# Kernel optimization log

Measured on AMD Instinct MI355X. Metric: run time of the kernel, lower is better.

## Reference

```python
import jax, jax.numpy as jnp
import numpy as np

B, H, E, G, SEQ_LEN = 131072, 64, 16, 32, 30


def setup_inputs() -> dict:
    key = jax.random.key(0)
    ks = jax.random.split(key, 17)
    def lin(kw, kb, out_f, in_f):
        s = 1.0 / np.sqrt(in_f)
        W = jax.random.uniform(kw, (out_f, in_f), jnp.float32, -s, s)
        b = jax.random.uniform(kb, (out_f,), jnp.float32, -s, s)
        return W, b
    W_se, b_se = lin(ks[0], ks[1], E, 2)
    W_h2p, b_h2p = lin(ks[2], ks[3], 2, 3 * H)
    W_goal, b_goal = lin(ks[4], ks[5], H, 2 * G)
    W_abs, b_abs = lin(ks[6], ks[7], H, 2)
    W_ih, b_ih = lin(ks[8], ks[9], 4 * H, E)
    W_hh, b_hh = lin(ks[10], ks[11], 4 * H, H)
    return {
        "traj_abs": jax.random.normal(ks[12], (1, B, 2), jnp.float32),
        "traj_rel": jax.random.normal(ks[13], (1, B, 2), jnp.float32),
        "h0": jax.random.normal(ks[14], (1, B, H), jnp.float32),
        "c0": jax.random.normal(ks[15], (1, B, H), jnp.float32),
        "goals": jax.random.normal(ks[16], (B, G, 2), jnp.float32),
        "W_ih": W_ih, "W_hh": W_hh, "b_ih": b_ih, "b_hh": b_hh,
        "W_se": W_se, "b_se": b_se,
        "W_h2p": W_h2p, "b_h2p": b_h2p,
        "W_goal": W_goal, "b_goal": b_goal,
        "W_abs": W_abs, "b_abs": b_abs,
    }


def reference(traj_abs, traj_rel, h0, c0, goals,
              W_ih, W_hh, b_ih, b_hh,
              W_se, b_se, W_h2p, b_h2p,
              W_goal, b_goal, W_abs, b_abs):
    b = traj_abs.shape[1]
    goal_emb = goals.reshape(b, -1) @ W_goal.T + b_goal            # (b, H)
    dec_in = jax.nn.leaky_relu(traj_rel[0] @ W_se.T + b_se)        # (b, E)

    def step(carry, _):
        h, c, x, abs_pos = carry
        gates = x @ W_ih.T + b_ih + h @ W_hh.T + b_hh              # (b, 4H)
        i, f, g, o = jnp.split(gates, 4, axis=-1)                  # PyTorch gate order
        c = jax.nn.sigmoid(f) * c + jax.nn.sigmoid(i) * jnp.tanh(g)
        h = jax.nn.sigmoid(o) * jnp.tanh(c)
        abs_emb = abs_pos @ W_abs.T + b_abs                        # (b, H)
        inp = jnp.concatenate([h, abs_emb, goal_emb], axis=1)      # (b, 3H)
        rel = inp @ W_h2p.T + b_h2p                                # (b, 2)
        x = jax.nn.leaky_relu(rel @ W_se.T + b_se)
        return (h, c, x, abs_pos + rel), rel

    _, rels = jax.lax.scan(step, (h0[0], c0[0], dec_in, traj_abs[0]),
                           None, length=SEQ_LEN)
    return rels  # (seq_len, b, 2)
```

## Files before the change

kernel.cpp:

```cpp
#include <hip/hip_runtime.h>
#include <stdint.h>


#define B_TOT 131072
#define SEQL 30
#define WPB 8

typedef _Float16 f16x8 __attribute__((ext_vector_type(8)));
typedef _Float16 f16x2 __attribute__((ext_vector_type(2)));
typedef float f32x4 __attribute__((ext_vector_type(4)));
typedef float f32x2 __attribute__((ext_vector_type(2)));

__device__ __forceinline__ float fexp2(float x) {
#if __has_builtin(__builtin_amdgcn_exp2f)
  return __builtin_amdgcn_exp2f(x);
#else
  return exp2f(x);
#endif
}
__device__ __forceinline__ float frcp(float x) {
#if __has_builtin(__builtin_amdgcn_rcpf)
  return __builtin_amdgcn_rcpf(x);
#else
  return 1.0f / x;
#endif
}

__global__ void setup_consts(const float* __restrict__ Wgoal,
                             const float* __restrict__ bgoal,
                             const float* __restrict__ Wh2p,
                             const float* __restrict__ bh2p,
                             const float* __restrict__ Wabs,
                             const float* __restrict__ babs,
                             float* __restrict__ wsf) {
  const int tid = threadIdx.x;
  const int wv = tid >> 6;
  const int lane = tid & 63;
  if (wv == 0) {
    const int k = lane;
    float s0 = 0.f, s1 = 0.f;
#pragma unroll 8
    for (int jj = 0; jj < 64; ++jj) {
      float wg = Wgoal[jj * 64 + k];
      s0 += wg * Wh2p[128 + jj];
      s1 += wg * Wh2p[320 + jj];
    }
    wsf[k] = s0;
    wsf[64 + k] = s1;
  } else {
    const int i = lane >> 3, sub = lane & 7;
    const int p = i & 1, grp = i >> 1;
    float s = 0.f;
#pragma unroll
    for (int t = 0; t < 8; ++t) {
      int j = sub * 8 + t;
      float wv_ = (grp < 3) ? Wh2p[p * 192 + 64 + j] : Wh2p[p * 192 + 128 + j];
      float av = (grp == 0)   ? Wabs[j * 2 + 0]
                 : (grp == 1) ? Wabs[j * 2 + 1]
                 : (grp == 2) ? babs[j]
                              : bgoal[j];
      s += av * wv_;
    }
    s += __shfl_xor(s, 1, 64);
    s += __shfl_xor(s, 2, 64);
    s += __shfl_xor(s, 4, 64);
    if (sub == 0) {
      if (grp == 2) s += bh2p[p];
      wsf[128 + i] = s;
    }
  }
}

__global__ __launch_bounds__(512, 4) void lstm_mfma(
    const float* __restrict__ tabs, const float* __restrict__ trel,
    const float* __restrict__ h0, const float* __restrict__ c0,
    const float* __restrict__ goals, const float* __restrict__ Wih,
    const float* __restrict__ Whh, const float* __restrict__ bih,
    const float* __restrict__ bhh, const float* __restrict__ Wse,
    const float* __restrict__ bse, const float* __restrict__ Wh2p,
    const float* __restrict__ wsf, float* __restrict__ outp) {
  const int lane = threadIdx.x & 63;
  const int w = threadIdx.x >> 6;
  const int q = lane >> 4;
  const int n = lane & 15;
  const int pm = n & 3;
  const int bb = blockIdx.x * (16 * WPB) + 16 * w;

  __shared__ __align__(16) _Float16 whh[4 * 64 * 64];
  __shared__ __align__(16) _Float16 wx[4 * 64 * 32];
  __shared__ __align__(16) _Float16 hscr[WPB * 16 * 64];

  const float SI = -1.4426950408889634f;
  const float SG = 2.8853900817779268f;

  for (int idx = threadIdx.x; idx < 4 * 64 * 64; idx += 512) {
    const int r = idx >> 6, k = idx & 63;
    const float sc = ((r >> 6) == 2) ? SG : SI;
    const int slot = (k >> 3) ^ (r & 7);
    whh[r * 64 + slot * 8 + (k & 7)] = (_Float16)(sc * Whh[r * 64 + k]);
  }
  if (threadIdx.x < 256) {
    const int r = threadIdx.x;
    const float sc = ((r >> 6) == 2) ? SG : SI;
    float bfold = 0.f, m20 = 0.f, m21 = 0.f;
#pragma unroll
    for (int k = 0; k < 16; ++k) {
      float wik = Wih[r * 16 + k];
      bfold += bse[k] * wik;
      m20 += Wse[k * 2 + 0] * wik;
      m21 += Wse[k * 2 + 1] * wik;
    }
    const float bias = sc * (bih[r] + bhh[r] + 0.505f * bfold);
#pragma unroll
    for (int kx = 0; kx < 32; ++kx) {
      float v;
      if (kx < 16)
        v = sc * Wih[r * 16 + kx];
      else if (kx == 16)
        v = bias;
      else if (kx == 17)
        v = sc * 0.505f * m20;
      else if (kx == 18)
        v = sc * 0.505f * m21;
      else
        v = 0.f;
      const int slot = (kx >> 3) ^ (r & 3);
      wx[r * 32 + slot * 8 + (kx & 7)] = (_Float16)v;
    }
  }

  f16x8 awp0, awp1;
#pragma unroll
  for (int j = 0; j < 8; ++j) {
    float v0 = (pm < 2) ? Wh2p[pm * 192 + q * 8 + j] : 0.f;
    float v1 = (pm < 2) ? Wh2p[pm * 192 + 32 + q * 8 + j] : 0.f;
    awp0[j] = (_Float16)v0;
    awp1[j] = (_Float16)v1;
  }
  const float Sx0 = wsf[128], Sx1 = wsf[129];
  const float Sy0 = wsf[130], Sy1 = wsf[131];

  f16x2 wsaP[4], wsbP[4], bscP[4];
  const uint32_t xmask = (q < 2) ? 0x7FFF7FFFu : 0xFFFFFFFFu;
#pragma unroll
  for (int jj = 0; jj < 4; ++jj) {
    f16x2 z = f16x2{(_Float16)0.f, (_Float16)0.f};
    if (q < 2) {
      int kx = q * 8 + 2 * jj;
      wsaP[jj] = f16x2{(_Float16)(0.495f * Wse[kx * 2 + 0]),
                       (_Float16)(0.495f * Wse[kx * 2 + 2])};
      wsbP[jj] = f16x2{(_Float16)(0.495f * Wse[kx * 2 + 1]),
                       (_Float16)(0.495f * Wse[kx * 2 + 3])};
      bscP[jj] = f16x2{(_Float16)(0.495f * bse[kx]),
                       (_Float16)(0.495f * bse[kx + 1])};
    } else if (q == 2 && jj == 0) {
      wsaP[jj] = f16x2{(_Float16)0.f, (_Float16)1.f};
      wsbP[jj] = z;
      bscP[jj] = f16x2{(_Float16)1.f, (_Float16)0.f};
    } else if (q == 2 && jj == 1) {
      wsaP[jj] = z;
      wsbP[jj] = f16x2{(_Float16)1.f, (_Float16)0.f};
      bscP[jj] = z;
    } else {
      wsaP[jj] = z;
      wsbP[jj] = z;
      bscP[jj] = z;
    }
  }

  auto build_x = [&](float r0f, float r1f) -> f16x8 {
    f16x2 r0h = f16x2{(_Float16)r0f, (_Float16)r0f};
    f16x2 r1h = f16x2{(_Float16)r1f, (_Float16)r1f};
    f16x8 xr;
#pragma unroll
    for (int jj = 0; jj < 4; ++jj) {
      f16x2 t = r0h * wsaP[jj] + (r1h * wsbP[jj] + bscP[jj]);
      uint32_t tu = __builtin_bit_cast(uint32_t, t) & xmask;
      f16x2 lr = __builtin_bit_cast(f16x2, tu);
      xr[2 * jj] = lr[0];
      xr[2 * jj + 1] = lr[1];
    }
    return xr;
  };

  const f32x4 zC = {0.f, 0.f, 0.f, 0.f};
  const int wbase = w * 1024;

  float Gg0, Gg1, ax, ay;
  float cst[4][4];
  f16x8 xf;
  {
    f16x8 aM0, aM1, bg0, bg1;
#pragma unroll
    for (int j = 0; j < 8; ++j) {
      int k = q * 8 + j;
      aM0[j] = (_Float16)((pm < 2) ? wsf[pm * 64 + k] : 0.f);
      aM1[j] = (_Float16)((pm < 2) ? wsf[pm * 64 + 32 + k] : 0.f);
      bg0[j] = (_Float16)goals[(bb + n) * 64 + k];
      bg1[j] = (_Float16)goals[(bb + n) * 64 + 32 + k];
    }
    f32x4 Ga = __builtin_amdgcn_mfma_f32_16x16x32_f16(aM0, bg0, zC, 0, 0, 0);
    Ga = __builtin_amdgcn_mfma_f32_16x16x32_f16(aM1, bg1, Ga, 0, 0, 0);
    Gg0 = Ga[0] + wsf[132] + wsf[134];
    Gg1 = Ga[1] + wsf[133] + wsf[135];

    ax = tabs[(bb + n) * 2 + 0];
    ay = tabs[(bb + n) * 2 + 1];
#pragma unroll
    for (int m = 0; m < 4; ++m) {
      const int c16 = 2 * m + (n >> 3);
#pragma unroll
      for (int r = 0; r < 4; ++r) {
        const int br = 4 * q + r;
        cst[m][r] = c0[(bb + br) * 64 + 16 * m + n];
        hscr[wbase + br * 64 + ((c16 ^ (br & 7)) << 3) + (n & 7)] =
            (_Float16)h0[(bb + br) * 64 + 16 * m + n];
      }
    }
    xf = build_x(trel[(bb + n) * 2 + 0], trel[(bb + n) * 2 + 1]);
  }

  __syncthreads();

  const int ro0 = wbase + n * 64 + ((q ^ (n & 7)) << 3);
  const int ro1 = wbase + n * 64 + (((4 + q) ^ (n & 7)) << 3);
  const int sl0 = (q ^ (n & 7)) << 3;
  const int sl1 = ((4 + q) ^ (n & 7)) << 3;
  const int xsl = (q ^ (n & 3)) << 3;
  const float K2 = 2.8853900817779268f;

  for (int s = 0; s <= SEQL; ++s) {
    const f16x8 ah0 = *(const f16x8*)(hscr + ro0);
    const f16x8 ah1 = *(const f16x8*)(hscr + ro1);

    if (s > 0) {
      f32x4 p = __builtin_amdgcn_mfma_f32_16x16x32_f16(awp0, ah0, zC, 0, 0, 0);
      p = __builtin_amdgcn_mfma_f32_16x16x32_f16(awp1, ah1, p, 0, 0, 0);
      float u0 = p[0] + Gg0 + fmaf(ax, Sx0, ay * Sy0);
      float u1 = p[1] + Gg1 + fmaf(ax, Sx1, ay * Sy1);
      ax += u0;
      ay += u1;
      if (lane < 16) {
        float2 v;
        v.x = u0;
        v.y = u1;
        ((float2*)outp)[(size_t)(s - 1) * B_TOT + bb + lane] = v;
      }
      xf = build_x(u0, u1);
    }

    if (s < SEQL) {
#pragma unroll
      for (int m = 0; m < 4; ++m) {
        const int hb = (16 * m + n) * 64;
        const int xb = (16 * m + n) * 32 + xsl;
        f32x4 acc[4];
#pragma unroll
        for (int g = 0; g < 4; ++g) {
          const f16x8 w0 = *(const f16x8*)(whh + g * 4096 + hb + sl0);
          const f16x8 w1 = *(const f16x8*)(whh + g * 4096 + hb + sl1);
          const f16x8 w2 = *(const f16x8*)(wx + g * 2048 + xb);
          f32x4 a = __builtin_amdgcn_mfma_f32_16x16x32_f16(ah0, w0, zC,
                                                           0, 0, 0);
          a = __builtin_amdgcn_mfma_f32_16x16x32_f16(ah1, w1, a, 0, 0, 0);
          a = __builtin_amdgcn_mfma_f32_16x16x32_f16(xf, w2, a, 0, 0, 0);
          acc[g] = a;
        }
        const int c16 = 2 * m + (n >> 3);
#pragma unroll
        for (int pr = 0; pr < 2; ++pr) {
          const int ra = 2 * pr, rb = 2 * pr + 1;
          f32x2 Av = {fexp2(acc[0][ra]), fexp2(acc[0][rb])};
          f32x2 Fv = {fexp2(acc[1][ra]), fexp2(acc[1][rb])};
          f32x2 Bv = {fexp2(acc[2][ra]), fexp2(acc[2][rb])};
          const f32x2 one = {1.f, 1.f};
          f32x2 t1 = Av + one;
          f32x2 t2 = Bv + one;
          f32x2 t3 = Fv + one;
          f32x2 t4 = Bv - one;
          f32x2 m1 = t1 * t2;
          f32x2 cs = {cst[m][ra], cst[m][rb]};
          f32x2 num = cs * m1 + t4 * t3;
          f32x2 den = m1 * t3;
          float Rc = frcp(den[0] * den[1]);
          float cc0 = num[0] * den[1] * Rc;
          float cc1 = num[1] * den[0] * Rc;
          cst[m][ra] = cc0;
          cst[m][rb] = cc1;
          f32x2 Cv = {fexp2(acc[3][ra]), fexp2(acc[3][rb])};
          f32x2 Dv = {fexp2(K2 * cc0), fexp2(K2 * cc1)};
          f32x2 hd = (Cv + one) * (Dv + one);
          f32x2 hnm = Dv - one;
          float Rh = frcp(hd[0] * hd[1]);
          float h0v = hnm[0] * hd[1] * Rh;
          float h1v = hnm[1] * hd[0] * Rh;
          const int bra = 4 * q + ra, brb = 4 * q + rb;
          hscr[wbase + bra * 64 + ((c16 ^ (bra & 7)) << 3) + (n & 7)] =
              (_Float16)h0v;
          hscr[wbase + brb * 64 + ((c16 ^ (brb & 7)) << 3) + (n & 7)] =
              (_Float16)h1v;
        }
      }
    }
  }
}

extern "C" void kernel_launch(void* const* d_in, const int* in_sizes, int n_in,
                              void* d_out, int out_size, void* d_ws,
                              size_t ws_size, hipStream_t stream) {
  (void)in_sizes; (void)n_in; (void)out_size; (void)ws_size;
  const float* tabs  = (const float*)d_in[0];
  const float* trel  = (const float*)d_in[1];
  const float* h0    = (const float*)d_in[2];
  const float* c0    = (const float*)d_in[3];
  const float* goals = (const float*)d_in[4];
  const float* Wih   = (const float*)d_in[5];
  const float* Whh   = (const float*)d_in[6];
  const float* bih   = (const float*)d_in[7];
  const float* bhh   = (const float*)d_in[8];
  const float* Wse   = (const float*)d_in[9];
  const float* bse   = (const float*)d_in[10];
  const float* Wh2p  = (const float*)d_in[11];
  const float* bh2p  = (const float*)d_in[12];
  const float* Wgoal = (const float*)d_in[13];
  const float* bgoal = (const float*)d_in[14];
  const float* Wabs  = (const float*)d_in[15];
  const float* babs  = (const float*)d_in[16];
  float* wsf = (float*)d_ws;

  setup_consts<<<dim3(1), dim3(128), 0, stream>>>(Wgoal, bgoal, Wh2p, bh2p,
                                                  Wabs, babs, wsf);
  lstm_mfma<<<dim3(B_TOT / (16 * WPB)), dim3(512), 0, stream>>>(
      tabs, trel, h0, c0, goals, Wih, Whh, bih, bhh, Wse, bse, Wh2p, wsf,
      (float*)d_out);
}
```

Before: 447.4 us.

## Pre-swizzle weights into MFMA fragment order and transpose gate MFMA operands

Stores the LSTM recurrent and input weights in shared memory already laid out as per-lane MFMA B-fragments, so each lane loads its operand with one contiguous 16-byte read and no XOR swizzle addressing. The gate MFMAs swap operand order so each lane's accumulator holds consecutive hidden units for one batch row. That lets the new h be packed into f16x4 and written with one vector store instead of scalar 16-bit stores. h0 and c0 are now loaded with vectorized contiguous reads, at the cost of a new, bank-conflict-sensitive shared-memory layout for hscr.

```diff
diff --git a/kernel.cpp b/kernel.cpp
--- a/kernel.cpp
+++ b/kernel.cpp
@@ -7,6 +7,7 @@
 #define WPB 8
 
 typedef _Float16 f16x8 __attribute__((ext_vector_type(8)));
+typedef _Float16 f16x4 __attribute__((ext_vector_type(4)));
 typedef _Float16 f16x2 __attribute__((ext_vector_type(2)));
 typedef float f32x4 __attribute__((ext_vector_type(4)));
 typedef float f32x2 __attribute__((ext_vector_type(2)));
@@ -86,47 +87,50 @@
   const int pm = n & 3;
   const int bb = blockIdx.x * (16 * WPB) + 16 * w;
 
-  __shared__ __align__(16) _Float16 whh[4 * 64 * 64];
-  __shared__ __align__(16) _Float16 wx[4 * 64 * 32];
-  __shared__ __align__(16) _Float16 hscr[WPB * 16 * 64];
+  __shared__ __align__(16) _Float16 wfrag[48 * 512];
+  __shared__ __align__(16) _Float16 hscr[WPB * 2 * 512];
 
   const float SI = -1.4426950408889634f;
   const float SG = 2.8853900817779268f;
 
-  for (int idx = threadIdx.x; idx < 4 * 64 * 64; idx += 512) {
-    const int r = idx >> 6, k = idx & 63;
-    const float sc = ((r >> 6) == 2) ? SG : SI;
-    const int slot = (k >> 3) ^ (r & 7);
-    whh[r * 64 + slot * 8 + (k & 7)] = (_Float16)(sc * Whh[r * 64 + k]);
-  }
-  if (threadIdx.x < 256) {
-    const int r = threadIdx.x;
-    const float sc = ((r >> 6) == 2) ? SG : SI;
-    float bfold = 0.f, m20 = 0.f, m21 = 0.f;
-#pragma unroll
-    for (int k = 0; k < 16; ++k) {
-      float wik = Wih[r * 16 + k];
-      bfold += bse[k] * wik;
-      m20 += Wse[k * 2 + 0] * wik;
-      m21 += Wse[k * 2 + 1] * wik;
-    }
-    const float bias = sc * (bih[r] + bhh[r] + 0.505f * bfold);
-#pragma unroll
-    for (int kx = 0; kx < 32; ++kx) {
-      float v;
-      if (kx < 16)
-        v = sc * Wih[r * 16 + kx];
-      else if (kx == 16)
-        v = bias;
-      else if (kx == 17)
-        v = sc * 0.505f * m20;
-      else if (kx == 18)
-        v = sc * 0.505f * m21;
-      else
-        v = 0.f;
-      const int slot = (kx >> 3) ^ (r & 3);
-      wx[r * 32 + slot * 8 + (kx & 7)] = (_Float16)v;
-    }
+  for (int f = (int)(threadIdx.x >> 6); f < 48; f += 8) {
+    const int which = f % 3, gs = f / 3;
+    const int g = gs >> 2, s = gs & 3;
+    const int row = g * 64 + 16 * s + n;
+    const float sc = (g == 2) ? SG : SI;
+    f16x8 v;
+    if (which < 2) {
+#pragma unroll
+      for (int j = 0; j < 8; ++j)
+        v[j] = (_Float16)(sc * Whh[row * 64 + which * 32 + 8 * q + j]);
+    } else {
+      float bfold = 0.f, m20 = 0.f, m21 = 0.f;
+#pragma unroll
+      for (int k = 0; k < 16; ++k) {
+        float wik = Wih[row * 16 + k];
+        bfold += bse[k] * wik;
+        m20 += Wse[k * 2 + 0] * wik;
+        m21 += Wse[k * 2 + 1] * wik;
+      }
+      const float bias = sc * (bih[row] + bhh[row] + 0.505f * bfold);
+#pragma unroll
+      for (int j = 0; j < 8; ++j) {
+        const int kx = 8 * q + j;
+        float vv;
+        if (kx < 16)
+          vv = sc * Wih[row * 16 + kx];
+        else if (kx == 16)
+          vv = bias;
+        else if (kx == 17)
+          vv = sc * 0.505f * m20;
+        else if (kx == 18)
+          vv = sc * 0.505f * m21;
+        else
+          vv = 0.f;
+        v[j] = (_Float16)vv;
+      }
+    }
+    *(f16x8*)(wfrag + f * 512 + lane * 8) = v;
   }
 
   f16x8 awp0, awp1;
@@ -184,7 +188,7 @@
   };
 
   const f32x4 zC = {0.f, 0.f, 0.f, 0.f};
-  const int wbase = w * 1024;
+  const int wb = w * 1024;
 
   float Gg0, Gg1, ax, ay;
   float cst[4][4];
@@ -207,31 +211,34 @@
     ax = tabs[(bb + n) * 2 + 0];
     ay = tabs[(bb + n) * 2 + 1];
 #pragma unroll
-    for (int m = 0; m < 4; ++m) {
-      const int c16 = 2 * m + (n >> 3);
-#pragma unroll
-      for (int r = 0; r < 4; ++r) {
-        const int br = 4 * q + r;
-        cst[m][r] = c0[(bb + br) * 64 + 16 * m + n];
-        hscr[wbase + br * 64 + ((c16 ^ (br & 7)) << 3) + (n & 7)] =
-            (_Float16)h0[(bb + br) * 64 + 16 * m + n];
-      }
+    for (int t = 0; t < 2; ++t) {
+      f16x8 hv;
+#pragma unroll
+      for (int j = 0; j < 8; ++j)
+        hv[j] = (_Float16)h0[(bb + n) * 64 + 32 * t + 8 * q + j];
+      *(f16x8*)(hscr + wb + t * 512 + lane * 8) = hv;
+    }
+#pragma unroll
+    for (int s4 = 0; s4 < 4; ++s4) {
+      const float4 cv =
+          *(const float4*)(c0 + (size_t)(bb + n) * 64 + 16 * s4 + 4 * q);
+      cst[s4][0] = cv.x;
+      cst[s4][1] = cv.y;
+      cst[s4][2] = cv.z;
+      cst[s4][3] = cv.w;
     }
     xf = build_x(trel[(bb + n) * 2 + 0], trel[(bb + n) * 2 + 1]);
   }
 
   __syncthreads();
 
-  const int ro0 = wbase + n * 64 + ((q ^ (n & 7)) << 3);
-  const int ro1 = wbase + n * 64 + (((4 + q) ^ (n & 7)) << 3);
-  const int sl0 = (q ^ (n & 7)) << 3;
-  const int sl1 = ((4 + q) ^ (n & 7)) << 3;
-  const int xsl = (q ^ (n & 3)) << 3;
+  const _Float16* wfp = wfrag + lane * 8;
+  const int wwo = wb + 128 * (q >> 1) + 8 * n + 4 * (q & 1);
   const float K2 = 2.8853900817779268f;
 
   for (int s = 0; s <= SEQL; ++s) {
-    const f16x8 ah0 = *(const f16x8*)(hscr + ro0);
-    const f16x8 ah1 = *(const f16x8*)(hscr + ro1);
+    const f16x8 ah0 = *(const f16x8*)(hscr + wb + lane * 8);
+    const f16x8 ah1 = *(const f16x8*)(hscr + wb + 512 + lane * 8);
 
     if (s > 0) {
       f32x4 p = __builtin_amdgcn_mfma_f32_16x16x32_f16(awp0, ah0, zC, 0, 0, 0);
@@ -251,22 +258,20 @@
 
     if (s < SEQL) {
 #pragma unroll
-      for (int m = 0; m < 4; ++m) {
-        const int hb = (16 * m + n) * 64;
-        const int xb = (16 * m + n) * 32 + xsl;
+      for (int s4 = 0; s4 < 4; ++s4) {
         f32x4 acc[4];
 #pragma unroll
         for (int g = 0; g < 4; ++g) {
-          const f16x8 w0 = *(const f16x8*)(whh + g * 4096 + hb + sl0);
-          const f16x8 w1 = *(const f16x8*)(whh + g * 4096 + hb + sl1);
-          const f16x8 w2 = *(const f16x8*)(wx + g * 2048 + xb);
-          f32x4 a = __builtin_amdgcn_mfma_f32_16x16x32_f16(ah0, w0, zC,
+          const f16x8 w0 = *(const f16x8*)(wfp + (12 * g + 3 * s4 + 0) * 512);
+          const f16x8 w1 = *(const f16x8*)(wfp + (12 * g + 3 * s4 + 1) * 512);
+          const f16x8 w2 = *(const f16x8*)(wfp + (12 * g + 3 * s4 + 2) * 512);
+          f32x4 a = __builtin_amdgcn_mfma_f32_16x16x32_f16(w0, ah0, zC,
                                                            0, 0, 0);
-          a = __builtin_amdgcn_mfma_f32_16x16x32_f16(ah1, w1, a, 0, 0, 0);
-          a = __builtin_amdgcn_mfma_f32_16x16x32_f16(xf, w2, a, 0, 0, 0);
+          a = __builtin_amdgcn_mfma_f32_16x16x32_f16(w1, ah1, a, 0, 0, 0);
+          a = __builtin_amdgcn_mfma_f32_16x16x32_f16(w2, xf, a, 0, 0, 0);
           acc[g] = a;
         }
-        const int c16 = 2 * m + (n >> 3);
+        f16x4 hp;
 #pragma unroll
         for (int pr = 0; pr < 2; ++pr) {
           const int ra = 2 * pr, rb = 2 * pr + 1;
@@ -279,27 +284,23 @@
           f32x2 t3 = Fv + one;
           f32x2 t4 = Bv - one;
           f32x2 m1 = t1 * t2;
-          f32x2 cs = {cst[m][ra], cst[m][rb]};
+          f32x2 cs = {cst[s4][ra], cst[s4][rb]};
           f32x2 num = cs * m1 + t4 * t3;
           f32x2 den = m1 * t3;
           float Rc = frcp(den[0] * den[1]);
           float cc0 = num[0] * den[1] * Rc;
           float cc1 = num[1] * den[0] * Rc;
-          cst[m][ra] = cc0;
-          cst[m][rb] = cc1;
+          cst[s4][ra] = cc0;
+          cst[s4][rb] = cc1;
           f32x2 Cv = {fexp2(acc[3][ra]), fexp2(acc[3][rb])};
           f32x2 Dv = {fexp2(K2 * cc0), fexp2(K2 * cc1)};
           f32x2 hd = (Cv + one) * (Dv + one);
           f32x2 hnm = Dv - one;
           float Rh = frcp(hd[0] * hd[1]);
-          float h0v = hnm[0] * hd[1] * Rh;
-          float h1v = hnm[1] * hd[0] * Rh;
-          const int bra = 4 * q + ra, brb = 4 * q + rb;
-          hscr[wbase + bra * 64 + ((c16 ^ (bra & 7)) << 3) + (n & 7)] =
-              (_Float16)h0v;
-          hscr[wbase + brb * 64 + ((c16 ^ (brb & 7)) << 3) + (n & 7)] =
-              (_Float16)h1v;
+          hp[ra] = (_Float16)(hnm[0] * hd[1] * Rh);
+          hp[rb] = (_Float16)(hnm[1] * hd[0] * Rh);
         }
+        *(f16x4*)(hscr + wwo + s4 * 256) = hp;
       }
     }
   }
```

New measurement: 478.9 us. 1.07x slower.
